# Kernel tuning notes

Measured on AMD Instinct MI355X. Metric: run time of the kernel, lower is better.

The kernel has to match this reference:

```python
import jax, jax.numpy as jnp
import numpy as np

B, N, D, L = 8, 2048, 256, 2  # batch, node_size, in_dim==mem_dim, num_layers


def setup_inputs() -> dict:
    key = jax.random.key(0)
    k_nodes, k_adj, k_w0, k_b0, k_wr, k_br = jax.random.split(key, 6)
    nodes = jax.random.normal(k_nodes, (B, N, D), dtype=jnp.float32)
    adj = jax.random.uniform(k_adj, (B, N, N), dtype=jnp.float32)
    s = 1.0 / np.sqrt(D)
    W0_w = jax.random.uniform(k_w0, (L, D, D), dtype=jnp.float32, minval=-s, maxval=s)
    W0_b = jax.random.uniform(k_b0, (L, D), dtype=jnp.float32, minval=-s, maxval=s)
    Wr_w = jax.random.uniform(k_wr, (L, D, D), dtype=jnp.float32, minval=-s, maxval=s)
    Wr_b = jax.random.uniform(k_br, (L, D), dtype=jnp.float32, minval=-s, maxval=s)
    return {"nodes": nodes, "adj": adj, "W0_w": W0_w, "W0_b": W0_b,
            "Wr_w": Wr_w, "Wr_b": Wr_b}


def reference(nodes, adj, W0_w, W0_b, Wr_w, Wr_b):
    # denom[b] = row-sum of adj[b] + 1  -> [B, N, 1]
    denom = jnp.sum(adj, axis=2, keepdims=True) + 1.0
    x = nodes  # dropout is identity in eval mode
    outputs = x
    for l in range(L):
        # W_r branch: aggregate neighbor-transformed features
        xWr = jnp.einsum('bnd,md->bnm', x, Wr_w[l]) + Wr_b[l]   # [B,N,D]
        AxW = jnp.einsum('bnk,bkd->bnd', adj, xWr)              # sparse mm equiv
        # W_0 self branch, fused norm + relu
        xW0 = jnp.einsum('bnd,md->bnm', x, W0_w[l]) + W0_b[l]
        x = jax.nn.relu((AxW + xW0) / denom)
    return outputs + x
```

## Files before the change

kernel.cpp:

```cpp
#include <hip/hip_runtime.h>

constexpr int B = 8;
constexpr int N = 2048;
constexpr int D = 256;
constexpr int L = 2;
constexpr int M = B * N;

typedef __bf16 bf16x8 __attribute__((ext_vector_type(8)));
typedef float  f32x4  __attribute__((ext_vector_type(4)));

static __device__ __forceinline__ unsigned short f2bf(float f) {
    union { float f; unsigned u; } v; v.f = f;
    unsigned r = v.u + 0x7fffu + ((v.u >> 16) & 1u);
    return (unsigned short)(r >> 16);
}

static __device__ __forceinline__ void gload16(const void* g, void* l) {
    __builtin_amdgcn_global_load_lds(
        (__attribute__((address_space(1))) void*)(g),
        (__attribute__((address_space(3))) void*)(l),
        16, 0, 0);
}

__global__ __launch_bounds__(256)
void denom_cast_kernel(const float* __restrict__ adj,
                       unsigned short* __restrict__ adjb,
                       float* __restrict__ rdenom,
                       float* __restrict__ rowsum) {
    const int wave = threadIdx.x >> 6;
    const int lane = threadIdx.x & 63;
    const int row  = blockIdx.x * 4 + wave;
    const float4* p = (const float4*)(adj + (size_t)row * N);
    ushort4* q = (ushort4*)(adjb + (size_t)row * N);
    float s = 0.f;
    #pragma unroll
    for (int i = 0; i < 8; ++i) {
        float4 v = p[lane + i * 64];
        s += (v.x + v.y) + (v.z + v.w);
        ushort4 o;
        o.x = f2bf(v.x); o.y = f2bf(v.y); o.z = f2bf(v.z); o.w = f2bf(v.w);
        q[lane + i * 64] = o;
    }
    #pragma unroll
    for (int off = 32; off > 0; off >>= 1) s += __shfl_down(s, off);
    if (lane == 0) {
        rowsum[row] = s;
        rdenom[row] = 1.0f / (s + 1.0f);
    }
}

__global__ __launch_bounds__(256)
void cast_nodes_kernel(const float* __restrict__ nodes,
                       unsigned short* __restrict__ nodesbf,
                       unsigned short* __restrict__ nodesT) {
    __shared__ unsigned short T[64][68];
    const int b  = blockIdx.z;
    const int n0 = blockIdx.y * 64;
    const int d0 = blockIdx.x * 64;
    const int t  = threadIdx.x;
    const int r  = t >> 2;
    const int c4 = t & 3;
    const float*    src = nodes   + ((size_t)b * N + n0) * D + d0;
    unsigned short* dst = nodesbf + ((size_t)b * N + n0) * D + d0;
    #pragma unroll
    for (int rep = 0; rep < 4; ++rep) {
        const int fc = c4 + rep * 4;
        float4 v = *(const float4*)(src + (size_t)r * D + fc * 4);
        ushort4 o;
        o.x = f2bf(v.x); o.y = f2bf(v.y); o.z = f2bf(v.z); o.w = f2bf(v.w);
        *(ushort4*)(dst + (size_t)r * D + fc * 4) = o;
        *(ushort4*)&T[r][fc * 4] = o;
    }
    __syncthreads();
    unsigned short* dstT = nodesT + ((size_t)b * D + d0) * N + n0;
    #pragma unroll
    for (int rep = 0; rep < 4; ++rep) {
        const int nc = c4 + rep * 4;
        ushort4 o;
        o.x = T[nc * 4 + 0][r];
        o.y = T[nc * 4 + 1][r];
        o.z = T[nc * 4 + 2][r];
        o.w = T[nc * 4 + 3][r];
        *(ushort4*)(dstT + (size_t)r * N + nc * 4) = o;
    }
}

__global__ __launch_bounds__(256)
void cast_w_kernel(const float* __restrict__ W0_w, const float* __restrict__ Wr_w,
                   unsigned short* __restrict__ W0b, unsigned short* __restrict__ Wrb) {
    const int i = blockIdx.x * 256 + threadIdx.x;
    float4 a = ((const float4*)W0_w)[i];
    ushort4 o0; o0.x = f2bf(a.x); o0.y = f2bf(a.y); o0.z = f2bf(a.z); o0.w = f2bf(a.w);
    ((ushort4*)W0b)[i] = o0;
    float4 c = ((const float4*)Wr_w)[i];
    ushort4 o1; o1.x = f2bf(c.x); o1.y = f2bf(c.y); o1.z = f2bf(c.z); o1.w = f2bf(c.w);
    ((ushort4*)Wrb)[i] = o1;
}

__global__ __launch_bounds__(256)
void big_mfma_kernel(const unsigned short* __restrict__ adjb,
                     const unsigned short* __restrict__ xT,
                     unsigned short* __restrict__ y) {
    __shared__ unsigned short As[16 * 512];
    __shared__ unsigned short Bs[8 * 512];

    const int b    = blockIdx.z;
    const int n0   = blockIdx.x * 64;
    const int m0   = blockIdx.y * 128;
    const int t    = threadIdx.x;
    const int w    = t >> 6;
    const int lane = t & 63;
    const int lrow = lane & 15;
    const int lk   = (lane >> 4) * 8;

    const unsigned short* Ab = adjb + (size_t)b * N * N;
    const unsigned short* Bb = xT   + (size_t)b * D * N;

    const unsigned short* gA0 = Ab + (size_t)(m0 + (2 * w + 0) * 16 + lrow) * N + lk;
    const unsigned short* gA1 = Ab + (size_t)(m0 + (2 * w + 1) * 16 + lrow) * N + lk;
    const unsigned short* gB  = Bb + (size_t)(n0 + w * 16 + lrow) * N + lk;

    f32x4 acc[4][2];
    const f32x4 zero = {0.f, 0.f, 0.f, 0.f};
    #pragma unroll
    for (int i = 0; i < 4; ++i)
        #pragma unroll
        for (int j = 0; j < 2; ++j) acc[i][j] = zero;

    for (int k0 = 0; k0 < N; k0 += 64) {
        __syncthreads();
        gload16(gA0 + k0,      &As[((2 * w + 0) * 2 + 0) * 512]);
        gload16(gA0 + k0 + 32, &As[((2 * w + 0) * 2 + 1) * 512]);
        gload16(gA1 + k0,      &As[((2 * w + 1) * 2 + 0) * 512]);
        gload16(gA1 + k0 + 32, &As[((2 * w + 1) * 2 + 1) * 512]);
        gload16(gB + k0,       &Bs[(w * 2 + 0) * 512]);
        gload16(gB + k0 + 32,  &Bs[(w * 2 + 1) * 512]);
        __syncthreads();
        #pragma unroll
        for (int kc = 0; kc < 2; ++kc) {
            bf16x8 a[4], bb[2];
            #pragma unroll
            for (int i = 0; i < 4; ++i) {
                const int mi = (w & 1) * 4 + i;
                a[i] = *(const bf16x8*)&As[(mi * 2 + kc) * 512 + lane * 8];
            }
            #pragma unroll
            for (int j = 0; j < 2; ++j) {
                const int ni = (w >> 1) * 2 + j;
                bb[j] = *(const bf16x8*)&Bs[(ni * 2 + kc) * 512 + lane * 8];
            }
            #pragma unroll
            for (int i = 0; i < 4; ++i)
                #pragma unroll
                for (int j = 0; j < 2; ++j)
                    acc[i][j] = __builtin_amdgcn_mfma_f32_16x16x32_bf16(
                        a[i], bb[j], acc[i][j], 0, 0, 0);
        }
    }

    unsigned short* yb = y + (size_t)b * N * D;
    const int col  = lane & 15;
    const int quad = lane >> 4;
    #pragma unroll
    for (int i = 0; i < 4; ++i) {
        const int mBase = m0 + (w & 1) * 64 + i * 16 + quad * 4;
        #pragma unroll
        for (int r = 0; r < 4; ++r) {
            const size_t rowOff = (size_t)(mBase + r) * D;
            #pragma unroll
            for (int j = 0; j < 2; ++j) {
                const int d = n0 + (w >> 1) * 32 + j * 16 + col;
                yb[rowOff + d] = f2bf(acc[i][j][r]);
            }
        }
    }
}

__global__ __launch_bounds__(256)
void small_mfma_kernel(const unsigned short* __restrict__ y,
                       const unsigned short* __restrict__ x,
                       const unsigned short* __restrict__ Wrb,
                       const unsigned short* __restrict__ W0b,
                       const float* __restrict__ br,
                       const float* __restrict__ b0,
                       const float* __restrict__ rdenom,
                       const float* __restrict__ rowsum,
                       const float* __restrict__ nodes,
                       unsigned short* __restrict__ xout,
                       unsigned short* __restrict__ xoutT,
                       float* __restrict__ out) {
    __shared__ unsigned short As[8 * 512];
    __shared__ unsigned short Bs[8 * 512];

    const int n0   = blockIdx.x * 64;
    const int m0   = blockIdx.y * 64;
    const int t    = threadIdx.x;
    const int w    = t >> 6;
    const int lane = t & 63;
    const int lrow = lane & 15;
    const int lk   = (lane >> 4) * 8;

    const size_t aRow = (size_t)(m0 + w * 16 + lrow) * D + lk;
    const size_t bRow = (size_t)(n0 + w * 16 + lrow) * D + lk;

    f32x4 acc[2][2];
    const f32x4 zero = {0.f, 0.f, 0.f, 0.f};
    #pragma unroll
    for (int i = 0; i < 2; ++i)
        #pragma unroll
        for (int j = 0; j < 2; ++j) acc[i][j] = zero;

    #pragma unroll
    for (int k0 = 0; k0 < 2 * D; k0 += 64) {
        const unsigned short* Ab = (k0 < D) ? y : x;
        const unsigned short* Bb = (k0 < D) ? Wrb : W0b;
        const int kk = k0 & (D - 1);
        __syncthreads();
        gload16(Ab + aRow + kk,      &As[(w * 2 + 0) * 512]);
        gload16(Ab + aRow + kk + 32, &As[(w * 2 + 1) * 512]);
        gload16(Bb + bRow + kk,      &Bs[(w * 2 + 0) * 512]);
        gload16(Bb + bRow + kk + 32, &Bs[(w * 2 + 1) * 512]);
        __syncthreads();
        #pragma unroll
        for (int kc = 0; kc < 2; ++kc) {
            bf16x8 a[2], bb[2];
            #pragma unroll
            for (int i = 0; i < 2; ++i)
                a[i] = *(const bf16x8*)&As[((((w & 1) * 2 + i) * 2) + kc) * 512 + lane * 8];
            #pragma unroll
            for (int j = 0; j < 2; ++j)
                bb[j] = *(const bf16x8*)&Bs[((((w >> 1) * 2 + j) * 2) + kc) * 512 + lane * 8];
            #pragma unroll
            for (int i = 0; i < 2; ++i)
                #pragma unroll
                for (int j = 0; j < 2; ++j)
                    acc[i][j] = __builtin_amdgcn_mfma_f32_16x16x32_bf16(
                        a[i], bb[j], acc[i][j], 0, 0, 0);
        }
    }

    const int col  = lane & 15;
    const int quad = lane >> 4;
    #pragma unroll
    for (int i = 0; i < 2; ++i) {
        const int mBase = m0 + (w & 1) * 32 + i * 16 + quad * 4;
        float rd[4], ss[4];
        #pragma unroll
        for (int r = 0; r < 4; ++r) {
            rd[r] = rdenom[mBase + r];
            ss[r] = rowsum[mBase + r];
        }
        #pragma unroll
        for (int j = 0; j < 2; ++j) {
            const int jj = n0 + (w >> 1) * 32 + j * 16 + col;
            const float bj = b0[jj];
            const float bv = br[jj];
            if (out) {
                #pragma unroll
                for (int r = 0; r < 4; ++r) {
                    const size_t idx = (size_t)(mBase + r) * D + jj;
                    float v = (acc[i][j][r] + bj + bv * ss[r]) * rd[r];
                    out[idx] = nodes[idx] + fmaxf(v, 0.f);
                }
            } else {
                ushort4 o;
                float v0 = fmaxf((acc[i][j][0] + bj + bv * ss[0]) * rd[0], 0.f);
                float v1 = fmaxf((acc[i][j][1] + bj + bv * ss[1]) * rd[1], 0.f);
                float v2 = fmaxf((acc[i][j][2] + bj + bv * ss[2]) * rd[2], 0.f);
                float v3 = fmaxf((acc[i][j][3] + bj + bv * ss[3]) * rd[3], 0.f);
                o.x = f2bf(v0); o.y = f2bf(v1); o.z = f2bf(v2); o.w = f2bf(v3);
                xout[(size_t)(mBase + 0) * D + jj] = o.x;
                xout[(size_t)(mBase + 1) * D + jj] = o.y;
                xout[(size_t)(mBase + 2) * D + jj] = o.z;
                xout[(size_t)(mBase + 3) * D + jj] = o.w;
                const int bb_ = m0 >> 11;
                const int nloc = mBase & (N - 1);
                *(ushort4*)&xoutT[((size_t)bb_ * D + jj) * N + nloc] = o;
            }
        }
    }
}

extern "C" void kernel_launch(void* const* d_in, const int* in_sizes, int n_in,
                              void* d_out, int out_size, void* d_ws, size_t ws_size,
                              hipStream_t stream) {
    const float* nodes = (const float*)d_in[0];
    const float* adj   = (const float*)d_in[1];
    const float* W0_w  = (const float*)d_in[2];
    const float* W0_b  = (const float*)d_in[3];
    const float* Wr_w  = (const float*)d_in[4];
    const float* Wr_b  = (const float*)d_in[5];
    float* out = (float*)d_out;

    unsigned short* adjb    = (unsigned short*)d_ws;
    unsigned short* xTbuf   = adjb  + (size_t)B * N * N;
    unsigned short* nodesbf = xTbuf + (size_t)B * D * N;
    unsigned short* ybuf    = nodesbf + (size_t)B * N * D;
    unsigned short* x1      = ybuf  + (size_t)B * N * D;
    unsigned short* Wrb     = x1    + (size_t)B * N * D;
    unsigned short* W0b     = Wrb   + (size_t)L * D * D;
    float* rdenom = (float*)(W0b + (size_t)L * D * D);
    float* rowsum = rdenom + M;

    denom_cast_kernel<<<dim3(B * N / 4), 256, 0, stream>>>(adj, adjb, rdenom, rowsum);
    cast_nodes_kernel<<<dim3(D / 64, N / 64, B), 256, 0, stream>>>(nodes, nodesbf, xTbuf);
    cast_w_kernel<<<dim3(L * D * D / 4 / 256), 256, 0, stream>>>(W0_w, Wr_w, W0b, Wrb);

    big_mfma_kernel<<<dim3(D / 64, N / 128, B), 256, 0, stream>>>(adjb, xTbuf, ybuf);
    small_mfma_kernel<<<dim3(D / 64, M / 64), 256, 0, stream>>>(
        ybuf, nodesbf, Wrb, W0b, Wr_b, W0_b, rdenom, rowsum,
        nullptr, x1, xTbuf, nullptr);

    big_mfma_kernel<<<dim3(D / 64, N / 128, B), 256, 0, stream>>>(adjb, xTbuf, ybuf);
    small_mfma_kernel<<<dim3(D / 64, M / 64), 256, 0, stream>>>(
        ybuf, x1, Wrb + D * D, W0b + D * D, Wr_b + D, W0_b + D, rdenom, rowsum,
        nodes, nullptr, nullptr, out);
}
```

Before: 362.3 us.

## Split-K adjacency GEMM with larger tiles, fold partial sums into small GEMM

The adjacency GEMM now uses 128x128 output tiles and splits the K dimension in two, writing two bf16 partial results. The small GEMM kernel consumes both partials as separate K stages against the same Wr weight, which performs the reduction algebraically, and its tile height is enlarged to 128. The final residual reads the bf16 copy of nodes instead of fp32. This aims to improve data reuse in the dominant GEMM while keeping parallelism, at the cost of extra partial-buffer traffic, an extra K pass, and added bf16 rounding error.

```diff
diff --git a/kernel.cpp b/kernel.cpp
--- a/kernel.cpp
+++ b/kernel.cpp
@@ -13,6 +13,11 @@
     union { float f; unsigned u; } v; v.f = f;
     unsigned r = v.u + 0x7fffu + ((v.u >> 16) & 1u);
     return (unsigned short)(r >> 16);
+}
+
+static __device__ __forceinline__ float bf2f(unsigned short u) {
+    union { unsigned u; float f; } v; v.u = ((unsigned)u) << 16;
+    return v.f;
 }
 
 static __device__ __forceinline__ void gload16(const void* g, void* l) {
@@ -100,11 +105,101 @@
 __global__ __launch_bounds__(256)
 void big_mfma_kernel(const unsigned short* __restrict__ adjb,
                      const unsigned short* __restrict__ xT,
-                     unsigned short* __restrict__ y) {
+                     unsigned short* __restrict__ ypart) {
+    __shared__ unsigned short As[16 * 512];
+    __shared__ unsigned short Bs[16 * 512];
+
+    const int z     = blockIdx.z;
+    const int b     = z & 7;
+    const int split = z >> 3;
+    const int n0    = blockIdx.x * 128;
+    const int m0    = blockIdx.y * 128;
+    const int t     = threadIdx.x;
+    const int w     = t >> 6;
+    const int lane  = t & 63;
+    const int lrow  = lane & 15;
+    const int lk    = (lane >> 4) * 8;
+    const int kbase = split * (N / 2);
+
+    const unsigned short* Ab = adjb + (size_t)b * N * N + kbase;
+    const unsigned short* Bb = xT   + (size_t)b * D * N + kbase;
+
+    const unsigned short* gA0 = Ab + (size_t)(m0 + (2 * w + 0) * 16 + lrow) * N + lk;
+    const unsigned short* gA1 = Ab + (size_t)(m0 + (2 * w + 1) * 16 + lrow) * N + lk;
+    const unsigned short* gB0 = Bb + (size_t)(n0 + (2 * w + 0) * 16 + lrow) * N + lk;
+    const unsigned short* gB1 = Bb + (size_t)(n0 + (2 * w + 1) * 16 + lrow) * N + lk;
+
+    f32x4 acc[4][4];
+    const f32x4 zero = {0.f, 0.f, 0.f, 0.f};
+    #pragma unroll
+    for (int i = 0; i < 4; ++i)
+        #pragma unroll
+        for (int j = 0; j < 4; ++j) acc[i][j] = zero;
+
+    for (int k0 = 0; k0 < N / 2; k0 += 64) {
+        __syncthreads();
+        gload16(gA0 + k0,      &As[((2 * w + 0) * 2 + 0) * 512]);
+        gload16(gA0 + k0 + 32, &As[((2 * w + 0) * 2 + 1) * 512]);
+        gload16(gA1 + k0,      &As[((2 * w + 1) * 2 + 0) * 512]);
+        gload16(gA1 + k0 + 32, &As[((2 * w + 1) * 2 + 1) * 512]);
+        gload16(gB0 + k0,      &Bs[((2 * w + 0) * 2 + 0) * 512]);
+        gload16(gB0 + k0 + 32, &Bs[((2 * w + 0) * 2 + 1) * 512]);
+        gload16(gB1 + k0,      &Bs[((2 * w + 1) * 2 + 0) * 512]);
+        gload16(gB1 + k0 + 32, &Bs[((2 * w + 1) * 2 + 1) * 512]);
+        __syncthreads();
+        #pragma unroll
+        for (int kc = 0; kc < 2; ++kc) {
+            bf16x8 a[4], bb[4];
+            #pragma unroll
+            for (int i = 0; i < 4; ++i)
+                a[i] = *(const bf16x8*)&As[((((w & 1) * 4 + i) * 2) + kc) * 512 + lane * 8];
+            #pragma unroll
+            for (int j = 0; j < 4; ++j)
+                bb[j] = *(const bf16x8*)&Bs[((((w >> 1) * 4 + j) * 2) + kc) * 512 + lane * 8];
+            #pragma unroll
+            for (int i = 0; i < 4; ++i)
+                #pragma unroll
+                for (int j = 0; j < 4; ++j)
+                    acc[i][j] = __builtin_amdgcn_mfma_f32_16x16x32_bf16(
+                        a[i], bb[j], acc[i][j], 0, 0, 0);
+        }
+    }
+
+    unsigned short* yb = ypart + ((size_t)split * M + (size_t)b * N) * D;
+    const int col  = lane & 15;
+    const int quad = lane >> 4;
+    #pragma unroll
+    for (int i = 0; i < 4; ++i) {
+        const int mBase = m0 + (w & 1) * 64 + i * 16 + quad * 4;
+        #pragma unroll
+        for (int r = 0; r < 4; ++r) {
+            const size_t rowOff = (size_t)(mBase + r) * D;
+            #pragma unroll
+            for (int j = 0; j < 4; ++j) {
+                const int d = n0 + (w >> 1) * 64 + j * 16 + col;
+                yb[rowOff + d] = f2bf(acc[i][j][r]);
+            }
+        }
+    }
+}
+
+__global__ __launch_bounds__(256)
+void small_mfma_kernel(const unsigned short* __restrict__ y0,
+                       const unsigned short* __restrict__ y1,
+                       const unsigned short* __restrict__ x,
+                       const unsigned short* __restrict__ Wrb,
+                       const unsigned short* __restrict__ W0b,
+                       const float* __restrict__ br,
+                       const float* __restrict__ b0,
+                       const float* __restrict__ rdenom,
+                       const float* __restrict__ rowsum,
+                       const unsigned short* __restrict__ nodesbf,
+                       unsigned short* __restrict__ xout,
+                       unsigned short* __restrict__ xoutT,
+                       float* __restrict__ out) {
     __shared__ unsigned short As[16 * 512];
     __shared__ unsigned short Bs[8 * 512];
 
-    const int b    = blockIdx.z;
     const int n0   = blockIdx.x * 64;
     const int m0   = blockIdx.y * 128;
     const int t    = threadIdx.x;
@@ -113,12 +208,9 @@
     const int lrow = lane & 15;
     const int lk   = (lane >> 4) * 8;
 
-    const unsigned short* Ab = adjb + (size_t)b * N * N;
-    const unsigned short* Bb = xT   + (size_t)b * D * N;
-
-    const unsigned short* gA0 = Ab + (size_t)(m0 + (2 * w + 0) * 16 + lrow) * N + lk;
-    const unsigned short* gA1 = Ab + (size_t)(m0 + (2 * w + 1) * 16 + lrow) * N + lk;
-    const unsigned short* gB  = Bb + (size_t)(n0 + w * 16 + lrow) * N + lk;
+    const size_t aRow0 = (size_t)(m0 + (2 * w + 0) * 16 + lrow) * D + lk;
+    const size_t aRow1 = (size_t)(m0 + (2 * w + 1) * 16 + lrow) * D + lk;
+    const size_t bRow  = (size_t)(n0 + w * 16 + lrow) * D + lk;
 
     f32x4 acc[4][2];
     const f32x4 zero = {0.f, 0.f, 0.f, 0.f};
@@ -127,123 +219,44 @@
         #pragma unroll
         for (int j = 0; j < 2; ++j) acc[i][j] = zero;
 
-    for (int k0 = 0; k0 < N; k0 += 64) {
-        __syncthreads();
-        gload16(gA0 + k0,      &As[((2 * w + 0) * 2 + 0) * 512]);
-        gload16(gA0 + k0 + 32, &As[((2 * w + 0) * 2 + 1) * 512]);
-        gload16(gA1 + k0,      &As[((2 * w + 1) * 2 + 0) * 512]);
-        gload16(gA1 + k0 + 32, &As[((2 * w + 1) * 2 + 1) * 512]);
-        gload16(gB + k0,       &Bs[(w * 2 + 0) * 512]);
-        gload16(gB + k0 + 32,  &Bs[(w * 2 + 1) * 512]);
-        __syncthreads();
-        #pragma unroll
-        for (int kc = 0; kc < 2; ++kc) {
-            bf16x8 a[4], bb[2];
-            #pragma unroll
-            for (int i = 0; i < 4; ++i) {
-                const int mi = (w & 1) * 4 + i;
-                a[i] = *(const bf16x8*)&As[(mi * 2 + kc) * 512 + lane * 8];
+    #pragma unroll
+    for (int s = 0; s < 3; ++s) {
+        const unsigned short* Asrc = (s == 0) ? y0 : (s == 1) ? y1 : x;
+        const unsigned short* Bsrc = (s < 2) ? Wrb : W0b;
+        #pragma unroll
+        for (int kk = 0; kk < D; kk += 64) {
+            __syncthreads();
+            gload16(Asrc + aRow0 + kk,      &As[((2 * w + 0) * 2 + 0) * 512]);
+            gload16(Asrc + aRow0 + kk + 32, &As[((2 * w + 0) * 2 + 1) * 512]);
+            gload16(Asrc + aRow1 + kk,      &As[((2 * w + 1) * 2 + 0) * 512]);
+            gload16(Asrc + aRow1 + kk + 32, &As[((2 * w + 1) * 2 + 1) * 512]);
+            gload16(Bsrc + bRow + kk,       &Bs[(w * 2 + 0) * 512]);
+            gload16(Bsrc + bRow + kk + 32,  &Bs[(w * 2 + 1) * 512]);
+            __syncthreads();
+            #pragma unroll
+            for (int kc = 0; kc < 2; ++kc) {
+                bf16x8 a[4], bb[2];
+                #pragma unroll
+                for (int i = 0; i < 4; ++i)
+                    a[i] = *(const bf16x8*)&As[((((w & 1) * 4 + i) * 2) + kc) * 512 + lane * 8];
+                #pragma unroll
+                for (int j = 0; j < 2; ++j)
+                    bb[j] = *(const bf16x8*)&Bs[((((w >> 1) * 2 + j) * 2) + kc) * 512 + lane * 8];
+                #pragma unroll
+                for (int i = 0; i < 4; ++i)
+                    #pragma unroll
+                    for (int j = 0; j < 2; ++j)
+                        acc[i][j] = __builtin_amdgcn_mfma_f32_16x16x32_bf16(
+                            a[i], bb[j], acc[i][j], 0, 0, 0);
             }
-            #pragma unroll
-            for (int j = 0; j < 2; ++j) {
-                const int ni = (w >> 1) * 2 + j;
-                bb[j] = *(const bf16x8*)&Bs[(ni * 2 + kc) * 512 + lane * 8];
-            }
-            #pragma unroll
-            for (int i = 0; i < 4; ++i)
-                #pragma unroll
-                for (int j = 0; j < 2; ++j)
-                    acc[i][j] = __builtin_amdgcn_mfma_f32_16x16x32_bf16(
-                        a[i], bb[j], acc[i][j], 0, 0, 0);
-        }
-    }
-
-    unsigned short* yb = y + (size_t)b * N * D;
+        }
+    }
+
     const int col  = lane & 15;
     const int quad = lane >> 4;
     #pragma unroll
     for (int i = 0; i < 4; ++i) {
         const int mBase = m0 + (w & 1) * 64 + i * 16 + quad * 4;
-        #pragma unroll
-        for (int r = 0; r < 4; ++r) {
-            const size_t rowOff = (size_t)(mBase + r) * D;
-            #pragma unroll
-            for (int j = 0; j < 2; ++j) {
-                const int d = n0 + (w >> 1) * 32 + j * 16 + col;
-                yb[rowOff + d] = f2bf(acc[i][j][r]);
-            }
-        }
-    }
-}
-
-__global__ __launch_bounds__(256)
-void small_mfma_kernel(const unsigned short* __restrict__ y,
-                       const unsigned short* __restrict__ x,
-                       const unsigned short* __restrict__ Wrb,
-                       const unsigned short* __restrict__ W0b,
-                       const float* __restrict__ br,
-                       const float* __restrict__ b0,
-                       const float* __restrict__ rdenom,
-                       const float* __restrict__ rowsum,
-                       const float* __restrict__ nodes,
-                       unsigned short* __restrict__ xout,
-                       unsigned short* __restrict__ xoutT,
-                       float* __restrict__ out) {
-    __shared__ unsigned short As[8 * 512];
-    __shared__ unsigned short Bs[8 * 512];
-
-    const int n0   = blockIdx.x * 64;
-    const int m0   = blockIdx.y * 64;
-    const int t    = threadIdx.x;
-    const int w    = t >> 6;
-    const int lane = t & 63;
-    const int lrow = lane & 15;
-    const int lk   = (lane >> 4) * 8;
-
-    const size_t aRow = (size_t)(m0 + w * 16 + lrow) * D + lk;
-    const size_t bRow = (size_t)(n0 + w * 16 + lrow) * D + lk;
-
-    f32x4 acc[2][2];
-    const f32x4 zero = {0.f, 0.f, 0.f, 0.f};
-    #pragma unroll
-    for (int i = 0; i < 2; ++i)
-        #pragma unroll
-        for (int j = 0; j < 2; ++j) acc[i][j] = zero;
-
-    #pragma unroll
-    for (int k0 = 0; k0 < 2 * D; k0 += 64) {
-        const unsigned short* Ab = (k0 < D) ? y : x;
-        const unsigned short* Bb = (k0 < D) ? Wrb : W0b;
-        const int kk = k0 & (D - 1);
-        __syncthreads();
-        gload16(Ab + aRow + kk,      &As[(w * 2 + 0) * 512]);
-        gload16(Ab + aRow + kk + 32, &As[(w * 2 + 1) * 512]);
-        gload16(Bb + bRow + kk,      &Bs[(w * 2 + 0) * 512]);
-        gload16(Bb + bRow + kk + 32, &Bs[(w * 2 + 1) * 512]);
-        __syncthreads();
-        #pragma unroll
-        for (int kc = 0; kc < 2; ++kc) {
-            bf16x8 a[2], bb[2];
-            #pragma unroll
-            for (int i = 0; i < 2; ++i)
-                a[i] = *(const bf16x8*)&As[((((w & 1) * 2 + i) * 2) + kc) * 512 + lane * 8];
-            #pragma unroll
-            for (int j = 0; j < 2; ++j)
-                bb[j] = *(const bf16x8*)&Bs[((((w >> 1) * 2 + j) * 2) + kc) * 512 + lane * 8];
-            #pragma unroll
-            for (int i = 0; i < 2; ++i)
-                #pragma unroll
-                for (int j = 0; j < 2; ++j)
-                    acc[i][j] = __builtin_amdgcn_mfma_f32_16x16x32_bf16(
-                        a[i], bb[j], acc[i][j], 0, 0, 0);
-        }
-    }
-
-    const int col  = lane & 15;
-    const int quad = lane >> 4;
-    #pragma unroll
-    for (int i = 0; i < 2; ++i) {
-        const int mBase = m0 + (w & 1) * 32 + i * 16 + quad * 4;
         float rd[4], ss[4];
         #pragma unroll
         for (int r = 0; r < 4; ++r) {
@@ -260,7 +273,7 @@
                 for (int r = 0; r < 4; ++r) {
                     const size_t idx = (size_t)(mBase + r) * D + jj;
                     float v = (acc[i][j][r] + bj + bv * ss[r]) * rd[r];
-                    out[idx] = nodes[idx] + fmaxf(v, 0.f);
+                    out[idx] = bf2f(nodesbf[idx]) + fmaxf(v, 0.f);
                 }
             } else {
                 ushort4 o;
@@ -296,8 +309,8 @@
     unsigned short* xTbuf   = adjb  + (size_t)B * N * N;
     unsigned short* nodesbf = xTbuf + (size_t)B * D * N;
     unsigned short* ybuf    = nodesbf + (size_t)B * N * D;
-    unsigned short* x1      = ybuf  + (size_t)B * N * D;
-    unsigned short* Wrb     = x1    + (size_t)B * N * D;
+    unsigned short* x1      = ybuf  + (size_t)2 * M * D;
+    unsigned short* Wrb     = x1    + (size_t)M * D;
     unsigned short* W0b     = Wrb   + (size_t)L * D * D;
     float* rdenom = (float*)(W0b + (size_t)L * D * D);
     float* rowsum = rdenom + M;
@@ -306,13 +319,16 @@
     cast_nodes_kernel<<<dim3(D / 64, N / 64, B), 256, 0, stream>>>(nodes, nodesbf, xTbuf);
     cast_w_kernel<<<dim3(L * D * D / 4 / 256), 256, 0, stream>>>(W0_w, Wr_w, W0b, Wrb);
 
-    big_mfma_kernel<<<dim3(D / 64, N / 128, B), 256, 0, stream>>>(adjb, xTbuf, ybuf);
-    small_mfma_kernel<<<dim3(D / 64, M / 64), 256, 0, stream>>>(
-        ybuf, nodesbf, Wrb, W0b, Wr_b, W0_b, rdenom, rowsum,
+    unsigned short* y0 = ybuf;
+    unsigned short* y1 = ybuf + (size_t)M * D;
+
+    big_mfma_kernel<<<dim3(D / 128, N / 128, 2 * B), 256, 0, stream>>>(adjb, xTbuf, ybuf);
+    small_mfma_kernel<<<dim3(D / 64, M / 128), 256, 0, stream>>>(
+        y0, y1, nodesbf, Wrb, W0b, Wr_b, W0_b, rdenom, rowsum,
         nullptr, x1, xTbuf, nullptr);
 
-    big_mfma_kernel<<<dim3(D / 64, N / 128, B), 256, 0, stream>>>(adjb, xTbuf, ybuf);
-    small_mfma_kernel<<<dim3(D / 64, M / 64), 256, 0, stream>>>(
-        ybuf, x1, Wrb + D * D, W0b + D * D, Wr_b + D, W0_b + D, rdenom, rowsum,
-        nodes, nullptr, nullptr, out);
-}
+    big_mfma_kernel<<<dim3(D / 128, N / 128, 2 * B), 256, 0, stream>>>(adjb, xTbuf, ybuf);
+    small_mfma_kernel<<<dim3(D / 64, M / 128), 256, 0, stream>>>(
+        y0, y1, x1, Wrb + D * D, W0b + D * D, Wr_b + D, W0_b + D, rdenom, rowsum,
+        nodesbf, nullptr, nullptr, out);
+}
```

Result: faster. 341.5 us (-5.7%).
